# Kernel tuning notes

Hardware: AMD Instinct MI355X
Metric: run time of the kernel (lower is better)

The kernel has to match this reference:

```python
import jax, jax.numpy as jnp
import numpy as np

EMBED_DIM = 512
NUM_HEADS = 8
NUM_RULES = 16
HEAD_DIM = EMBED_DIM // NUM_HEADS


def setup_inputs() -> dict:
    key = jax.random.key(0)
    ks = jax.random.split(key, 10)
    B, S, E, H, R, D = 4, 2048, EMBED_DIM, NUM_HEADS, NUM_RULES, HEAD_DIM
    lim_q = 1.0 / np.sqrt(E)
    lim_v = 1.0 / np.sqrt(E)
    return {
        "query": jax.random.normal(ks[0], (B, S, E), jnp.float32),
        "key": jax.random.normal(ks[1], (B, S, E), jnp.float32),
        "value": jax.random.normal(ks[2], (B, S, E), jnp.float32),
        "Wq": jax.random.uniform(ks[3], (E, E), jnp.float32, -lim_q, lim_q),
        "bq": jax.random.uniform(ks[4], (E,), jnp.float32, -lim_q, lim_q),
        "Wv": jax.random.uniform(ks[5], (E * R, E), jnp.float32, -lim_v, lim_v),
        "bv": jax.random.uniform(ks[6], (E * R,), jnp.float32, -lim_v, lim_v),
        "Wo": jax.random.uniform(ks[7], (E, E), jnp.float32, -lim_q, lim_q),
        "bo": jax.random.uniform(ks[8], (E,), jnp.float32, -lim_q, lim_q),
        "rules_keys": 0.02 * jax.random.normal(ks[9], (H, R, D), jnp.float32),
        "rules_widths": jnp.ones((H, R, D), jnp.float32),
    }


def reference(query, key, value, Wq, bq, Wv, bv, Wo, bo, rules_keys, rules_widths):
    B, S, E = query.shape
    H, R, D = NUM_HEADS, NUM_RULES, HEAD_DIM
    scale = D ** -0.5
    # preprocessing_query: Linear + scale, split heads -> (b, h, s, d)
    q = (query @ Wq.T + bq) * scale
    q = q.reshape(B, S, H, D).transpose(0, 2, 1, 3)
    # custom_distance (l1): |q - rule_key| broadcast over rules -> (b, h, s, r, d)
    diff = jnp.abs(q[:, :, :, None, :] - rules_keys[None, :, None, :, :])
    # get_z_values: z = mean_d( -0.5 * (diff / width)^2 ) -> (b, h, s, r)
    z = -0.5 * jnp.mean(jnp.square(diff / rules_widths[None, :, None, :, :]), axis=-1)
    # softmax over rules (last dim), dropout is identity (p=0)
    attn = jax.nn.softmax(z, axis=-1)  # (b, h, s, r)
    # preprocessing_value: Linear(E -> E*R) + scale, 'b s (h d r) -> b s h d r'
    v = (value @ Wv.T + bv) * scale
    v = v.reshape(B, S, H, D, R)
    # Fnn_output = attn * v summed over rules -> (b, s, h, d)
    out = jnp.einsum("bhsr,bshdr->bshd", attn, v)
    # torch: (b,s,h,d).transpose(1,2).contiguous().view(b, -1, h*d)
    out = out.transpose(0, 2, 1, 3).reshape(B, -1, H * D)
    return out @ Wo.T + bo
```

## Files before the change

### kernel.cpp

```cpp
#include <hip/hip_runtime.h>
#include <stdint.h>

#define TOKENS 8192
#define EDIM 512
#define HNUM 8
#define RNUM 16
#define DDIM 64
#define KDIM 512

typedef short v8s __attribute__((ext_vector_type(8)));
typedef float v4f __attribute__((ext_vector_type(4)));

__device__ inline unsigned short f2b(float f) {
    union { float f; unsigned int i; } c; c.f = f;
    unsigned int i = c.i + 0x7fffu + ((c.i >> 16) & 1u);
    return (unsigned short)(i >> 16);
}

#define GLD16(dst, src) \
    __builtin_amdgcn_global_load_lds((__attribute__((address_space(1))) void*)(src), \
                                     (__attribute__((address_space(3))) void*)(dst), 16, 0, 0)

__global__ __launch_bounds__(256)
void cvt5(const float* __restrict__ s0, const float* __restrict__ s1,
          const float* __restrict__ s2, const float* __restrict__ s3,
          const float* __restrict__ s4,
          unsigned short* __restrict__ d0, unsigned short* __restrict__ d1,
          unsigned short* __restrict__ d2, unsigned short* __restrict__ d3,
          unsigned short* __restrict__ d4,
          int n0, int n1, int n2, int n3, int n4)
{
    const float* s; unsigned short* d; int n;
    switch (blockIdx.y) {
        case 0: s = s0; d = d0; n = n0; break;
        case 1: s = s1; d = d1; n = n1; break;
        case 2: s = s2; d = d2; n = n2; break;
        case 3: s = s3; d = d3; n = n3; break;
        default: s = s4; d = d4; n = n4; break;
    }
    size_t base = (size_t)blockIdx.x * 2048 + (size_t)threadIdx.x * 8;
    if (base >= (size_t)n) return;
    const float4* sp = (const float4*)(s + base);
    float4 f0 = sp[0], f1 = sp[1];
    v8s o;
    o[0] = (short)f2b(f0.x); o[1] = (short)f2b(f0.y);
    o[2] = (short)f2b(f0.z); o[3] = (short)f2b(f0.w);
    o[4] = (short)f2b(f1.x); o[5] = (short)f2b(f1.y);
    o[6] = (short)f2b(f1.z); o[7] = (short)f2b(f1.w);
    *(v8s*)(d + base) = o;
}

template <int MODE>
__global__ __launch_bounds__(256, 2)
void gemm_bt(const unsigned short* __restrict__ A,
             const unsigned short* __restrict__ B,
             const float* __restrict__ bias,
             float* __restrict__ outF,
             unsigned short* __restrict__ outH,
             const float* __restrict__ attn)
{
    __shared__ unsigned short As[128 * 32];
    __shared__ unsigned short Bs[128 * 32];

    const int tid  = threadIdx.x;
    const int w    = tid >> 6;
    const int lane = tid & 63;
    const int quad = lane >> 4;
    const int l16  = lane & 15;
    const int wm   = w >> 1, wn = w & 1;
    const int m0   = blockIdx.x * 128;
    const int n0   = blockIdx.y * 128;

    v4f acc[4][4];
#pragma unroll
    for (int i = 0; i < 4; ++i)
#pragma unroll
        for (int j = 0; j < 4; ++j)
            acc[i][j] = (v4f){0.f, 0.f, 0.f, 0.f};

    for (int kt = 0; kt < KDIM / 32; ++kt) {
#pragma unroll
        for (int p = 0; p < 2; ++p) {
            int cb = w * 128 + p * 64;
            int c  = cb + lane;
            const unsigned short* sa = A + (size_t)(m0 + (c >> 2)) * KDIM + kt * 32 + (c & 3) * 8;
            GLD16(&As[cb * 8], sa);
            const unsigned short* sb = B + (size_t)(n0 + (c >> 2)) * KDIM + kt * 32 + (c & 3) * 8;
            GLD16(&Bs[cb * 8], sb);
        }
        __syncthreads();

        v8s af[4], bf[4];
#pragma unroll
        for (int mt = 0; mt < 4; ++mt)
            af[mt] = *(const v8s*)&As[(wm * 64 + mt * 16 + l16) * 32 + quad * 8];
#pragma unroll
        for (int nt = 0; nt < 4; ++nt)
            bf[nt] = *(const v8s*)&Bs[(wn * 64 + nt * 16 + l16) * 32 + quad * 8];
#pragma unroll
        for (int mt = 0; mt < 4; ++mt)
#pragma unroll
            for (int nt = 0; nt < 4; ++nt)
                acc[mt][nt] = __builtin_amdgcn_mfma_f32_16x16x32_bf16(af[mt], bf[nt], acc[mt][nt], 0, 0, 0);
        __syncthreads();
    }

    if (MODE == 1) {
#pragma unroll
        for (int nt = 0; nt < 4; ++nt) {
            int col = n0 + wn * 64 + nt * 16 + l16;
            int h   = col >> 10;
            int d   = (col >> 4) & 63;
            float bvv = bias[col];
#pragma unroll
            for (int mt = 0; mt < 4; ++mt) {
                int rowb = m0 + wm * 64 + mt * 16 + quad * 4;
#pragma unroll
                for (int rg = 0; rg < 4; ++rg) {
                    int token = rowb + rg;
                    float av = attn[(size_t)token * (HNUM * RNUM) + h * RNUM + l16];
                    float v  = (acc[mt][nt][rg] + bvv) * av;
                    v += __shfl_xor(v, 1);
                    v += __shfl_xor(v, 2);
                    v += __shfl_xor(v, 4);
                    v += __shfl_xor(v, 8);
                    if (l16 == 0) {
                        int g = (token >> 11) * 2048 + h * 256 + ((token & 2047) >> 3);
                        int j = ((token & 7) << 6) + d;
                        outH[(size_t)g * EDIM + j] = f2b(v * 0.125f);
                    }
                }
            }
        }
    } else {
#pragma unroll
        for (int mt = 0; mt < 4; ++mt)
#pragma unroll
            for (int nt = 0; nt < 4; ++nt) {
                int col = n0 + wn * 64 + nt * 16 + l16;
                float bb = bias[col];
#pragma unroll
                for (int rg = 0; rg < 4; ++rg) {
                    int row = m0 + wm * 64 + mt * 16 + quad * 4 + rg;
                    float v = acc[mt][nt][rg] + bb;
                    if (MODE == 0) outF[(size_t)row * EDIM + col] = v * 0.125f;
                    else           outF[(size_t)row * EDIM + col] = v;
                }
            }
    }
}

__global__ __launch_bounds__(256)
void rules_softmax(const float* __restrict__ q,
                   const float* __restrict__ rk,
                   const float* __restrict__ rw,
                   float* __restrict__ attn)
{
    __shared__ float rkf[RNUM * DDIM];
    __shared__ float iw2[RNUM * DDIM];
    const int h   = blockIdx.y;
    const int tid = threadIdx.x;
#pragma unroll
    for (int i = 0; i < 4; ++i) {
        int j = tid + i * 256;
        rkf[j] = rk[h * (RNUM * DDIM) + j];
        float iw = 1.0f / rw[h * (RNUM * DDIM) + j];
        iw2[j] = iw * iw;
    }
    __syncthreads();

    const int token = blockIdx.x * 256 + tid;
    const float4* qb = (const float4*)(q + (size_t)token * EDIM + h * DDIM);
    float z[RNUM];
#pragma unroll
    for (int r = 0; r < RNUM; ++r) z[r] = 0.f;
#pragma unroll
    for (int d4 = 0; d4 < DDIM / 4; ++d4) {
        float4 qv = qb[d4];
        float qs[4] = {qv.x, qv.y, qv.z, qv.w};
#pragma unroll
        for (int jj = 0; jj < 4; ++jj) {
            int d = d4 * 4 + jj;
#pragma unroll
            for (int r = 0; r < RNUM; ++r) {
                float t = qs[jj] - rkf[r * DDIM + d];
                z[r] += t * t * iw2[r * DDIM + d];
            }
        }
    }
    float mx = -1e30f;
#pragma unroll
    for (int r = 0; r < RNUM; ++r) {
        z[r] *= (-0.5f / 64.f);
        mx = fmaxf(mx, z[r]);
    }
    float s = 0.f;
#pragma unroll
    for (int r = 0; r < RNUM; ++r) { z[r] = __expf(z[r] - mx); s += z[r]; }
    float inv = 1.0f / s;
    float* ap = attn + (size_t)token * (HNUM * RNUM) + h * RNUM;
#pragma unroll
    for (int r = 0; r < RNUM; ++r) ap[r] = z[r] * inv;
}

extern "C" void kernel_launch(void* const* d_in, const int* in_sizes, int n_in,
                              void* d_out, int out_size, void* d_ws, size_t ws_size,
                              hipStream_t stream) {
    const float* query = (const float*)d_in[0];
    const float* value = (const float*)d_in[2];
    const float* Wq = (const float*)d_in[3];
    const float* bq = (const float*)d_in[4];
    const float* Wv = (const float*)d_in[5];
    const float* bv = (const float*)d_in[6];
    const float* Wo = (const float*)d_in[7];
    const float* bo = (const float*)d_in[8];
    const float* rk = (const float*)d_in[9];
    const float* rw = (const float*)d_in[10];

    char* ws = (char*)d_ws;
    unsigned short* qbf  = (unsigned short*)(ws);
    unsigned short* vbf  = (unsigned short*)(ws + (size_t)( 8 << 20));
    unsigned short* Wqb  = (unsigned short*)(ws + (size_t)(16 << 20));
    unsigned short* Wvb  = (unsigned short*)(ws + (size_t)(17 << 20));
    unsigned short* Wob  = (unsigned short*)(ws + (size_t)(25 << 20));
    unsigned short* out1 = (unsigned short*)(ws + (size_t)(26 << 20));
    float* qf            = (float*)(ws + (size_t)(34 << 20));
    float* attn          = (float*)(ws + (size_t)(50 << 20));

    dim3 blk(256);
    cvt5<<<dim3(2048, 5), blk, 0, stream>>>(query, value, Wv, Wq, Wo,
                                            qbf, vbf, Wvb, Wqb, Wob,
                                            TOKENS * EDIM, TOKENS * EDIM, EDIM * RNUM * EDIM,
                                            EDIM * EDIM, EDIM * EDIM);
    gemm_bt<0><<<dim3(TOKENS / 128, EDIM / 128), blk, 0, stream>>>(qbf, Wqb, bq, qf, nullptr, nullptr);
    rules_softmax<<<dim3(TOKENS / 256, HNUM), blk, 0, stream>>>(qf, rk, rw, attn);
    gemm_bt<1><<<dim3(TOKENS / 128, (EDIM * RNUM) / 128), blk, 0, stream>>>(vbf, Wvb, bv, nullptr, out1, attn);
    gemm_bt<2><<<dim3(TOKENS / 128, EDIM / 128), blk, 0, stream>>>(out1, Wob, bo, (float*)d_out, nullptr, nullptr);
}
```

Measured before the change: 274.3 us.

## Transpose value GEMM operands, stage epilogue in LDS, store q as bf16

The value-projection GEMM now swaps its operands so that rules lie along the accumulator register dimension. The rule reduction becomes a 4-element in-register dot product plus two cross-quad shuffles, and results are staged in LDS for 16-byte vectorized stores. Before, each element needed a 16-lane shuffle reduction and issued scattered 2-byte stores. The Q projection now writes bf16 instead of fp32. The rules softmax is rewritten to use one thread per (token, rule) with LDS-staged operands and shuffle-based softmax, trading extra precision loss in q for fewer bytes moved and better parallelism.

```diff
diff --git a/kernel.cpp b/kernel.cpp
--- a/kernel.cpp
+++ b/kernel.cpp
@@ -11,6 +11,9 @@
 typedef short v8s __attribute__((ext_vector_type(8)));
 typedef float v4f __attribute__((ext_vector_type(4)));
 
+__device__ inline float b2f(unsigned short u) {
+    union { unsigned int i; float f; } c; c.i = ((unsigned int)u) << 16; return c.f;
+}
 __device__ inline unsigned short f2b(float f) {
     union { float f; unsigned int i; } c; c.f = f;
     unsigned int i = c.i + 0x7fffu + ((c.i >> 16) & 1u);
@@ -61,6 +64,7 @@
 {
     __shared__ unsigned short As[128 * 32];
     __shared__ unsigned short Bs[128 * 32];
+    __shared__ unsigned short Os[128 * 8];
 
     const int tid  = threadIdx.x;
     const int w    = tid >> 6;
@@ -106,31 +110,35 @@
     }
 
     if (MODE == 1) {
+        const int h  = m0 >> 10;
+        const int d0 = (m0 >> 4) & 63;
+        float4 bias4[4];
+#pragma unroll
+        for (int mt = 0; mt < 4; ++mt)
+            bias4[mt] = *(const float4*)&bias[m0 + wm * 64 + mt * 16 + quad * 4];
 #pragma unroll
         for (int nt = 0; nt < 4; ++nt) {
-            int col = n0 + wn * 64 + nt * 16 + l16;
-            int h   = col >> 10;
-            int d   = (col >> 4) & 63;
-            float bvv = bias[col];
+            int token = n0 + wn * 64 + nt * 16 + l16;
+            float4 av = *(const float4*)&attn[(size_t)token * (HNUM * RNUM) + h * RNUM + quad * 4];
 #pragma unroll
             for (int mt = 0; mt < 4; ++mt) {
-                int rowb = m0 + wm * 64 + mt * 16 + quad * 4;
-#pragma unroll
-                for (int rg = 0; rg < 4; ++rg) {
-                    int token = rowb + rg;
-                    float av = attn[(size_t)token * (HNUM * RNUM) + h * RNUM + l16];
-                    float v  = (acc[mt][nt][rg] + bvv) * av;
-                    v += __shfl_xor(v, 1);
-                    v += __shfl_xor(v, 2);
-                    v += __shfl_xor(v, 4);
-                    v += __shfl_xor(v, 8);
-                    if (l16 == 0) {
-                        int g = (token >> 11) * 2048 + h * 256 + ((token & 2047) >> 3);
-                        int j = ((token & 7) << 6) + d;
-                        outH[(size_t)g * EDIM + j] = f2b(v * 0.125f);
-                    }
-                }
+                v4f a = acc[mt][nt];
+                float val = (a[0] + bias4[mt].x) * av.x
+                          + (a[1] + bias4[mt].y) * av.y
+                          + (a[2] + bias4[mt].z) * av.z
+                          + (a[3] + bias4[mt].w) * av.w;
+                val += __shfl_xor(val, 16);
+                val += __shfl_xor(val, 32);
+                if (quad == 0)
+                    Os[(wn * 64 + nt * 16 + l16) * 8 + (wm * 4 + mt)] = f2b(val * 0.125f);
             }
+        }
+        __syncthreads();
+        if (tid < 128) {
+            int sg = n0 + tid;
+            int g  = (sg >> 11) * 2048 + h * 256 + ((sg & 2047) >> 3);
+            int j  = (sg & 7) * 64 + d0;
+            *(v8s*)&outH[(size_t)g * EDIM + j] = *(const v8s*)&Os[tid * 8];
         }
     } else {
 #pragma unroll
@@ -143,64 +151,72 @@
                 for (int rg = 0; rg < 4; ++rg) {
                     int row = m0 + wm * 64 + mt * 16 + quad * 4 + rg;
                     float v = acc[mt][nt][rg] + bb;
-                    if (MODE == 0) outF[(size_t)row * EDIM + col] = v * 0.125f;
+                    if (MODE == 0) outH[(size_t)row * EDIM + col] = f2b(v * 0.125f);
                     else           outF[(size_t)row * EDIM + col] = v;
                 }
             }
     }
 }
 
+#define RST 72
 __global__ __launch_bounds__(256)
-void rules_softmax(const float* __restrict__ q,
+void rules_softmax(const unsigned short* __restrict__ q,
                    const float* __restrict__ rk,
                    const float* __restrict__ rw,
                    float* __restrict__ attn)
 {
-    __shared__ float rkf[RNUM * DDIM];
-    __shared__ float iw2[RNUM * DDIM];
+    __shared__ float ql[16 * RST];
+    __shared__ float rkl[16 * RST];
+    __shared__ float iwl[16 * RST];
     const int h   = blockIdx.y;
+    const int t0  = blockIdx.x * 16;
     const int tid = threadIdx.x;
+
 #pragma unroll
     for (int i = 0; i < 4; ++i) {
-        int j = tid + i * 256;
-        rkf[j] = rk[h * (RNUM * DDIM) + j];
-        float iw = 1.0f / rw[h * (RNUM * DDIM) + j];
-        iw2[j] = iw * iw;
+        int jj = tid + i * 256;
+        int r = jj >> 6, d = jj & 63;
+        rkl[r * RST + d] = rk[h * (RNUM * DDIM) + jj];
+        float wv = rw[h * (RNUM * DDIM) + jj];
+        iwl[r * RST + d] = 1.0f / (wv * wv);
+    }
+    {
+        int jj = tid * 4;
+        int row = jj >> 6, d = jj & 63;
+        const unsigned short* src = q + (size_t)(t0 + row) * EDIM + h * DDIM + d;
+        unsigned short u0 = src[0], u1 = src[1], u2 = src[2], u3 = src[3];
+        ql[row * RST + d + 0] = b2f(u0);
+        ql[row * RST + d + 1] = b2f(u1);
+        ql[row * RST + d + 2] = b2f(u2);
+        ql[row * RST + d + 3] = b2f(u3);
     }
     __syncthreads();
 
-    const int token = blockIdx.x * 256 + tid;
-    const float4* qb = (const float4*)(q + (size_t)token * EDIM + h * DDIM);
-    float z[RNUM];
-#pragma unroll
-    for (int r = 0; r < RNUM; ++r) z[r] = 0.f;
-#pragma unroll
-    for (int d4 = 0; d4 < DDIM / 4; ++d4) {
-        float4 qv = qb[d4];
-        float qs[4] = {qv.x, qv.y, qv.z, qv.w};
-#pragma unroll
-        for (int jj = 0; jj < 4; ++jj) {
-            int d = d4 * 4 + jj;
-#pragma unroll
-            for (int r = 0; r < RNUM; ++r) {
-                float t = qs[jj] - rkf[r * DDIM + d];
-                z[r] += t * t * iw2[r * DDIM + d];
-            }
-        }
-    }
-    float mx = -1e30f;
-#pragma unroll
-    for (int r = 0; r < RNUM; ++r) {
-        z[r] *= (-0.5f / 64.f);
-        mx = fmaxf(mx, z[r]);
-    }
-    float s = 0.f;
-#pragma unroll
-    for (int r = 0; r < RNUM; ++r) { z[r] = __expf(z[r] - mx); s += z[r]; }
-    float inv = 1.0f / s;
-    float* ap = attn + (size_t)token * (HNUM * RNUM) + h * RNUM;
-#pragma unroll
-    for (int r = 0; r < RNUM; ++r) ap[r] = z[r] * inv;
+    const int tl = tid >> 4;
+    const int r  = tid & 15;
+    const float* qrow = &ql[tl * RST];
+    const float* krow = &rkl[r * RST];
+    const float* wrow = &iwl[r * RST];
+    float z = 0.f;
+#pragma unroll
+    for (int d4 = 0; d4 < 16; ++d4) {
+        float4 qv = *(const float4*)&qrow[d4 * 4];
+        float4 kv = *(const float4*)&krow[d4 * 4];
+        float4 wv = *(const float4*)&wrow[d4 * 4];
+        float a0 = qv.x - kv.x; z += a0 * a0 * wv.x;
+        float a1 = qv.y - kv.y; z += a1 * a1 * wv.y;
+        float a2 = qv.z - kv.z; z += a2 * a2 * wv.z;
+        float a3 = qv.w - kv.w; z += a3 * a3 * wv.w;
+    }
+    z *= (-0.5f / 64.f);
+    float mx = z;
+#pragma unroll
+    for (int s = 1; s < 16; s <<= 1) mx = fmaxf(mx, __shfl_xor(mx, s));
+    float e = __expf(z - mx);
+    float sum = e;
+#pragma unroll
+    for (int s = 1; s < 16; s <<= 1) sum += __shfl_xor(sum, s);
+    attn[(size_t)(t0 + tl) * (HNUM * RNUM) + h * RNUM + r] = e / sum;
 }
 
 extern "C" void kernel_launch(void* const* d_in, const int* in_sizes, int n_in,
@@ -224,16 +240,16 @@
     unsigned short* Wvb  = (unsigned short*)(ws + (size_t)(17 << 20));
     unsigned short* Wob  = (unsigned short*)(ws + (size_t)(25 << 20));
     unsigned short* out1 = (unsigned short*)(ws + (size_t)(26 << 20));
-    float* qf            = (float*)(ws + (size_t)(34 << 20));
-    float* attn          = (float*)(ws + (size_t)(50 << 20));
+    unsigned short* qf   = (unsigned short*)(ws + (size_t)(34 << 20));
+    float* attn          = (float*)(ws + (size_t)(42 << 20));
 
     dim3 blk(256);
     cvt5<<<dim3(2048, 5), blk, 0, stream>>>(query, value, Wv, Wq, Wo,
                                             qbf, vbf, Wvb, Wqb, Wob,
                                             TOKENS * EDIM, TOKENS * EDIM, EDIM * RNUM * EDIM,
                                             EDIM * EDIM, EDIM * EDIM);
-    gemm_bt<0><<<dim3(TOKENS / 128, EDIM / 128), blk, 0, stream>>>(qbf, Wqb, bq, qf, nullptr, nullptr);
-    rules_softmax<<<dim3(TOKENS / 256, HNUM), blk, 0, stream>>>(qf, rk, rw, attn);
-    gemm_bt<1><<<dim3(TOKENS / 128, (EDIM * RNUM) / 128), blk, 0, stream>>>(vbf, Wvb, bv, nullptr, out1, attn);
+    gemm_bt<0><<<dim3(TOKENS / 128, EDIM / 128), blk, 0, stream>>>(qbf, Wqb, bq, nullptr, qf, nullptr);
+    rules_softmax<<<dim3(TOKENS / 16, HNUM), blk, 0, stream>>>(qf, rk, rw, attn);
+    gemm_bt<1><<<dim3((EDIM * RNUM) / 128, TOKENS / 128), blk, 0, stream>>>(Wvb, vbf, bv, nullptr, out1, attn);
     gemm_bt<2><<<dim3(TOKENS / 128, EDIM / 128), blk, 0, stream>>>(out1, Wob, bo, (float*)d_out, nullptr, nullptr);
 }
```

After: 241.7 us. 11.9% less time.
